# Kernel tuning notes

Measured on AMD Instinct MI355X. Metric: run time of the kernel, lower is better.

The kernel has to match this reference:

```python
import jax, jax.numpy as jnp
import numpy as np

B, N, C_IN, G = 8, 65536, 16, 64
CH = [16, 16]
EPS = 1e-3  # keras BatchNormalization default epsilon
OFFSETS = [(dx, dy, dz) for dx in (-1, 0, 1) for dy in (-1, 0, 1) for dz in (-1, 0, 1)]
G3 = G * G * G


def setup_inputs() -> dict:
    key = jax.random.key(0)
    k = jax.random.split(key, 8)
    voxel_features = jax.random.normal(k[0], (B, N, C_IN), dtype=jnp.float32)
    # unique active voxel coordinates per example (submanifold sites)
    lin = jax.vmap(lambda kk: jax.random.permutation(kk, G3)[:N])(jax.random.split(k[1], B))
    xyz = jnp.stack([lin // (G * G), (lin // G) % G, lin % G], axis=-1).astype(jnp.int32)
    num_valid_voxels = jax.random.randint(k[2], (B,), N // 2, N + 1).astype(jnp.int32)
    w0 = jax.random.uniform(k[3], (3, 3, 3, C_IN, CH[0]), minval=-0.05, maxval=0.05, dtype=jnp.float32)
    w1 = jax.random.uniform(k[4], (3, 3, 3, CH[0], CH[1]), minval=-0.05, maxval=0.05, dtype=jnp.float32)
    nw0 = jax.random.uniform(k[5], (3, 3, 3, 1, 1), minval=-0.05, maxval=0.05, dtype=jnp.float32)
    nw1 = jax.random.uniform(k[6], (3, 3, 3, 1, 1), minval=-0.05, maxval=0.05, dtype=jnp.float32)
    gamma0 = jnp.ones((CH[0],), jnp.float32); beta0 = jnp.zeros((CH[0],), jnp.float32)
    gamma1 = jnp.ones((CH[1],), jnp.float32); beta1 = jnp.zeros((CH[1],), jnp.float32)
    return dict(voxel_features=voxel_features, voxel_xyz_indices=xyz,
                num_valid_voxels=num_valid_voxels, w0=w0, w1=w1, nw0=nw0, nw1=nw1,
                gamma0=gamma0, beta0=beta0, gamma1=gamma1, beta1=beta1)


def build_neighbor_idx(coords, valid_mask):
    """For each voxel and each 3x3x3 offset, the row index of the active neighbor, or -1."""
    lin = coords[..., 0] * (G * G) + coords[..., 1] * G + coords[..., 2]  # [B,N]
    # invalid (padded) voxels write to a spare slot so they never match as neighbors
    write_lin = jnp.where(valid_mask, lin, G3 + 1)
    idx_map = jnp.full((B, G3 + 2), -1, jnp.int32)
    idx_map = idx_map.at[jnp.arange(B)[:, None], write_lin].set(
        jnp.broadcast_to(jnp.arange(N, dtype=jnp.int32)[None, :], (B, N)))
    brow = jnp.arange(B)[:, None]
    nb = []
    for dx, dy, dz in OFFSETS:
        nx = coords[..., 0] + dx; ny = coords[..., 1] + dy; nz = coords[..., 2] + dz
        inb = (nx >= 0) & (nx < G) & (ny >= 0) & (ny < G) & (nz >= 0) & (nz < G)
        nlin = jnp.where(inb, nx * (G * G) + ny * G + nz, G3)  # slot G3 always -1
        nb.append(idx_map[brow, nlin])
    return jnp.stack(nb, axis=1)  # [B,27,N]


def sparse_conv(feats, nb_idx, valid_mask, w):
    """Submanifold sparse 3D conv: output only at active sites, gathering active neighbors."""
    wf = w.reshape(27, w.shape[3], w.shape[4])  # offsets enumerate kernel taps in order
    out = jnp.zeros((feats.shape[0], feats.shape[1], w.shape[4]), feats.dtype)
    for o in range(27):
        idx = nb_idx[:, o]  # [B,N]
        g = jnp.take_along_axis(feats, jnp.maximum(idx, 0)[..., None], axis=1)
        g = jnp.where((idx >= 0)[..., None], g, 0.0)
        out = out + jnp.einsum('bnc,co->bno', g, wf[o])
    return out * valid_mask[..., None]


def masked_bn(x, valid_mask, num_valid, gamma, beta):
    m = valid_mask[..., None].astype(x.dtype)
    cnt = jnp.sum(num_valid).astype(x.dtype)
    mean = jnp.sum(x * m, axis=(0, 1)) / cnt
    var = jnp.sum(m * jnp.square(x - mean), axis=(0, 1)) / cnt
    xn = (x - mean) * jax.lax.rsqrt(var + EPS) * gamma + beta
    return xn * m  # padded rows are zero-padded, as in the TF layer


def reference(voxel_features, voxel_xyz_indices, num_valid_voxels,
              w0, w1, nw0, nw1, gamma0, beta0, gamma1, beta1):
    valid_mask = jnp.arange(N)[None, :] < num_valid_voxels[:, None]  # [B,N]
    nb_idx = build_neighbor_idx(voxel_xyz_indices, valid_mask)
    ones = jnp.ones((B, N, 1), jnp.float32)
    net = voxel_features
    for w, nw, g, b in ((w0, nw0, gamma0, beta0), (w1, nw1, gamma1, beta1)):
        net = sparse_conv(net, nb_idx, valid_mask, w)
        net_norm = sparse_conv(ones, nb_idx, valid_mask, nw)
        net = net / (1.0 + jnp.abs(net_norm))
        net = masked_bn(net, valid_mask, num_valid_voxels, g, b)
        net = jax.nn.relu(net)
    return net
```

## Files before the change

### kernel.cpp

```cpp
#include <hip/hip_runtime.h>
#include <cstdint>
#include <cstddef>

#define NB 8
#define NN 65536
#define NS (NN + 16)
#define GG 64
#define GG3 (GG*GG*GG)
#define NW (GG3/32)
#define NBLKC 2048
#define EPSC 1e-3f

typedef __bf16 bf16x8 __attribute__((ext_vector_type(8)));
typedef float  f32x4  __attribute__((ext_vector_type(4)));

__device__ __forceinline__ unsigned short f2bf(float f) {
    unsigned u = __builtin_bit_cast(unsigned, f);
    unsigned r = (u + 0x7fffu + ((u >> 16) & 1u)) >> 16;
    return (unsigned short)r;
}
__device__ __forceinline__ unsigned pk2(float a, float b) {
    return (unsigned)f2bf(a) | ((unsigned)f2bf(b) << 16);
}
__device__ __forceinline__ float bf2f(unsigned short s) {
    return __builtin_bit_cast(float, (unsigned)s << 16);
}

__device__ __forceinline__ int site_rank2(const int2* __restrict__ mwb, int lin) {
    int2 mw = mwb[lin >> 5];
    uint32_t w = (uint32_t)mw.x;
    uint32_t bit = 1u << (lin & 31);
    if (!(w & bit)) return -1;
    return mw.y + __popc(w & (bit - 1u));
}

__global__ __launch_bounds__(1024) void mask_scan_kernel(
    const int* __restrict__ xyz, const int* __restrict__ nvv,
    int2* __restrict__ mwb,
    const float* __restrict__ w0, const float* __restrict__ w1,
    unsigned short* __restrict__ wf,
    float* __restrict__ stats1, float* __restrict__ stats2)
{
    __shared__ uint32_t lmask[NW];
    __shared__ int wsum[16];
    __shared__ int woff[16];
    int b = blockIdx.x;
    int t = threadIdx.x;
    int lane = t & 63, wv = t >> 6;

    #pragma unroll
    for (int i = 0; i < NW / 1024; i++) lmask[t + i * 1024] = 0u;
    if (b == 0 && t < 512) { stats1[t] = 0.f; stats2[t] = 0.f; }
    __syncthreads();

    int cnt = nvv[b];
    const int* xb = xyz + (size_t)b * NN * 3;
    #pragma unroll 8
    for (int n = t; n < cnt; n += 1024) {
        const int* cp = xb + n * 3;
        int lin = cp[0] * (GG * GG) + cp[1] * GG + cp[2];
        atomicOr(&lmask[lin >> 5], 1u << (lin & 31));
    }
    __syncthreads();

    uint32_t wvv[8];
    int cnts[8];
    int local = 0;
    #pragma unroll
    for (int i = 0; i < 8; i++) {
        wvv[i] = lmask[i * 1024 + t];
        cnts[i] = __popc(wvv[i]);
        local += cnts[i];
    }

    int inc = local;
    #pragma unroll
    for (int d = 1; d < 64; d <<= 1) {
        int vtmp = __shfl_up(inc, d, 64);
        if (lane >= d) inc += vtmp;
    }
    if (lane == 63) wsum[wv] = inc;
    __syncthreads();
    if (t < 16) {
        int s = wsum[t];
        int e = s;
        #pragma unroll
        for (int d = 1; d < 16; d <<= 1) {
            int vtmp = __shfl_up(e, d, 16);
            if ((t & 15) >= d) e += vtmp;
        }
        woff[t] = e - s;
    }
    __syncthreads();

    int base = woff[wv] + (inc - local);
    int2* wb = mwb + (size_t)b * NW;
    #pragma unroll
    for (int i = 0; i < 8; i++) {
        wb[i * 1024 + t] = make_int2((int)wvv[i], base);
        base += cnts[i];
    }

    if (b < 2) {
        const float* w = b ? w1 : w0;
        unsigned short* o = wf + b * 14 * 512;
        for (int idx = t; idx < 14 * 512; idx += 1024) {
            int i = idx >> 9;
            int rem = idx & 511;
            int L = rem >> 3, j = rem & 7;
            int quad = L >> 4, nn = L & 15;
            int off = 2 * i + (quad >> 1);
            int c = ((quad & 1) << 3) + j;
            float v = (off < 27) ? w[(off * 16 + c) * 16 + nn] : 0.f;
            o[idx] = f2bf(v);
        }
    }
}

__global__ __launch_bounds__(256) void perm_gather_kernel(
    const int* __restrict__ xyz, const int* __restrict__ nvv,
    const int2* __restrict__ mwb,
    const float* __restrict__ feats,
    int2* __restrict__ srow,
    unsigned short* __restrict__ sfeats,
    int* __restrict__ rinv)
{
    int b = blockIdx.y;
    int n = blockIdx.x * 256 + threadIdx.x;
    int cnt = nvv[b];
    unsigned short* sfb = sfeats + (size_t)b * NS * 16;
    if (blockIdx.x == 0 && threadIdx.x < 16)
        sfb[(size_t)NN * 16 + threadIdx.x] = 0;
    if (n < cnt) {
        const int* cp = xyz + ((size_t)b * NN + n) * 3;
        int lin = cp[0] * (GG * GG) + cp[1] * GG + cp[2];
        int r = site_rank2(mwb + (size_t)b * NW, lin);
        srow[(size_t)b * NN + r] = make_int2(lin, n);
        rinv[(size_t)b * NN + n] = r;
        const float4* fp = (const float4*)(feats + ((size_t)b * NN + n) * 16);
        float4 f0 = fp[0], f1 = fp[1], f2 = fp[2], f3 = fp[3];
        uint4 lo = make_uint4(pk2(f0.x, f0.y), pk2(f0.z, f0.w),
                              pk2(f1.x, f1.y), pk2(f1.z, f1.w));
        uint4 hi = make_uint4(pk2(f2.x, f2.y), pk2(f2.z, f2.w),
                              pk2(f3.x, f3.y), pk2(f3.z, f3.w));
        *(uint4*)(sfb + (size_t)r * 16)     = lo;
        *(uint4*)(sfb + (size_t)r * 16 + 8) = hi;
    }
}

__global__ __launch_bounds__(256, 4) void conv_mfma_kernel(
    const unsigned short* __restrict__ sfeats,
    const int2*     __restrict__ srow,
    const int*      __restrict__ nvv,
    const int2*     __restrict__ mwb,
    const unsigned short* __restrict__ wfrag,
    const float*    __restrict__ nw,
    unsigned short* __restrict__ outbuf,
    float*          __restrict__ stats)
{
    int lane = threadIdx.x & 63;
    int wv = threadIdx.x >> 6;
    int m = lane & 15, quad = lane >> 4;
    int v = lane & 31, h = lane >> 5;

    int b    = blockIdx.x & 7;
    int widb = (blockIdx.x >> 3) * 4 + wv;

    __shared__ int   jj[4][32][29];
    __shared__ float rrl[4][32];
    __shared__ float red[4][32];
    __shared__ float lnw[27];

    if (threadIdx.x < 27) lnw[threadIdx.x] = nw[threadIdx.x];

    bf16x8 bfr[14];
    #pragma unroll
    for (int i = 0; i < 14; i++)
        bfr[i] = *(const bf16x8*)(wfrag + i * 512 + lane * 8);
    __syncthreads();

    float psum = 0.f, psq = 0.f;
    int coff = (quad & 1) << 3;

    int cnt = nvv[b];
    const int2* mb = mwb + (size_t)b * NW;
    const unsigned short* fb = sfeats + (size_t)b * NS * 16;
    const int2* sr = srow + (size_t)b * NN;

    int lin_nxt = sr[(widb << 5) + v].x;

    #pragma unroll 1
    for (int k = 0; k < 2; k++) {
        int r0 = (widb + k * 1024) << 5;
        int lin = lin_nxt;

        if (k == 0) {
            int Rv1 = r0 + (1024 << 5) + v;
            lin_nxt = (Rv1 < cnt) ? sr[Rv1].x : 0;
        }

        if (r0 >= cnt) continue;

        bool vld = (r0 + v) < cnt;
        if (!vld) lin = 0;
        int x = lin >> 12, y = (lin >> 6) & 63, z = lin & 63;
        int zb = z & 31;
        float nc = 0.f;
        #pragma unroll
        for (int t = 0; t < 5; t++) {
            int c = 2 * t + h;
            bool cok = c < 9;
            int cc = cok ? c : 0;
            int dx = cc / 3 - 1, dy = cc % 3 - 1;
            int nx = x + dx, ny = y + dy;
            bool colok = cok & ((unsigned)nx < 64u) & ((unsigned)ny < 64u);
            int wdi = colok ? (((nx << 12) + (ny << 6) + z) >> 5) : 0;

            int2 mw = make_int2(0, 0);
            if (vld & colok) mw = mb[wdi];
            bool need2 = vld & colok & (((zb == 0) & (z > 0)) | ((zb == 31) & (z < 63)));
            int w2 = wdi + ((zb == 0) ? -1 : 1);
            int2 mw2 = make_int2(0, 0);
            if (need2) mw2 = mb[w2];

            #pragma unroll
            for (int dz = -1; dz <= 1; dz++) {
                int zz = z + dz;
                bool zok = (unsigned)zz < 64u;
                bool same = (dz == 0) | ((dz < 0) ? (zb != 0) : (zb != 31));
                int2 word = same ? mw : mw2;
                int bb = zz & 31;
                uint32_t wm = (uint32_t)word.x;
                bool hit = vld & colok & zok & ((wm >> bb) & 1u);
                int rnk = word.y + __popc(wm & ((1u << bb) - 1u));
                int off = cc * 3 + dz + 1;
                int jv = hit ? rnk : NN;
                if (cok) {
                    jj[wv][v][off] = jv;
                    nc += hit ? lnw[off] : 0.f;
                }
            }
        }
        nc += __shfl_xor(nc, 32, 64);
        if (lane < 32) rrl[wv][v] = 1.f / (1.f + fabsf(nc));

        f32x4 acc0 = {0.f, 0.f, 0.f, 0.f};
        f32x4 acc1 = {0.f, 0.f, 0.f, 0.f};
        #pragma unroll
        for (int i = 0; i < 14; i++) {
            int off = 2 * i + (quad >> 1);
            int idx = off < 27 ? off : 28;
            int j0 = jj[wv][m][idx];      j0 = (off < 27) ? j0 : NN;
            int j1 = jj[wv][m + 16][idx]; j1 = (off < 27) ? j1 : NN;
            bf16x8 a0 = *(const bf16x8*)(fb + (size_t)j0 * 16 + coff);
            bf16x8 a1 = *(const bf16x8*)(fb + (size_t)j1 * 16 + coff);
            acc0 = __builtin_amdgcn_mfma_f32_16x16x32_bf16(a0, bfr[i], acc0, 0, 0, 0);
            acc1 = __builtin_amdgcn_mfma_f32_16x16x32_bf16(a1, bfr[i], acc1, 0, 0, 0);
        }

        #pragma unroll
        for (int hh = 0; hh < 2; hh++) {
            int rbase = r0 + (hh << 4);
            #pragma unroll
            for (int r4 = 0; r4 < 4; r4++) {
                int row = (quad << 2) + r4;
                float tval = (hh ? acc1[r4] : acc0[r4]) * rrl[wv][(hh << 4) + row];
                psum += tval; psq += tval * tval;
                int Rr = rbase + row;
                if (Rr < cnt)
                    outbuf[((size_t)b * NN + Rr) * 16 + m] = f2bf(tval);
            }
        }
    }

    psum += __shfl_xor(psum, 16, 64); psum += __shfl_xor(psum, 32, 64);
    psq  += __shfl_xor(psq, 16, 64);  psq  += __shfl_xor(psq, 32, 64);
    if (lane < 16) { red[wv][lane] = psum; red[wv][16 + lane] = psq; }
    __syncthreads();
    if (threadIdx.x < 32) {
        float vv = red[0][threadIdx.x] + red[1][threadIdx.x] +
                   red[2][threadIdx.x] + red[3][threadIdx.x];
        atomicAdd(&stats[(blockIdx.x & 15) * 32 + threadIdx.x], vv);
    }
}

__device__ __forceinline__ void compute_sb(
    const float* __restrict__ stats, const int* __restrict__ nvv,
    const float* __restrict__ gamma, const float* __restrict__ beta,
    float* sbs , float* sums )
{
    int tid = threadIdx.x;
    if (tid < 32) {
        float v = 0.f;
        #pragma unroll
        for (int s = 0; s < 16; s++) v += stats[s * 32 + tid];
        sums[tid] = v;
    }
    __syncthreads();
    if (tid < 16) {
        float cnt = 0.f;
        #pragma unroll
        for (int b = 0; b < NB; b++) cnt += (float)nvv[b];
        float mean = sums[tid] / cnt;
        float var  = fmaxf(sums[16 + tid] / cnt - mean * mean, 0.f);
        float scv = gamma[tid] * rsqrtf(var + EPSC);
        sbs[tid]      = scv;
        sbs[16 + tid] = beta[tid] - mean * scv;
    }
    __syncthreads();
}

__global__ __launch_bounds__(256) void bnrelu_sorted_kernel(
    const unsigned short* __restrict__ in, const float* __restrict__ stats,
    const int* __restrict__ nvv,
    const float* __restrict__ gamma, const float* __restrict__ beta,
    unsigned short* __restrict__ outb)
{
    __shared__ float sbs[32];
    __shared__ float sums[32];
    compute_sb(stats, nvv, gamma, beta, sbs, sums);

    int b = blockIdx.y;
    int r = blockIdx.x * 256 + threadIdx.x;
    if (r > NN) return;
    int cnt = nvv[b];
    if (r >= cnt && r != NN) return;
    uint4 lo = make_uint4(0, 0, 0, 0), hi = lo;
    if (r < cnt) {
        const uint4* ip = (const uint4*)(in + ((size_t)b * NN + r) * 16);
        uint4 xl = ip[0], xh = ip[1];
        float y[16];
        #pragma unroll
        for (int c = 0; c < 16; c++) {
            unsigned u = (c < 8) ? ((const unsigned*)&xl)[c >> 1]
                                 : ((const unsigned*)&xh)[(c - 8) >> 1];
            unsigned short sv = (c & 1) ? (unsigned short)(u >> 16)
                                        : (unsigned short)(u & 0xffff);
            y[c] = fmaxf(fmaf(bf2f(sv), sbs[c], sbs[16 + c]), 0.f);
        }
        lo = make_uint4(pk2(y[0], y[1]), pk2(y[2], y[3]), pk2(y[4], y[5]), pk2(y[6], y[7]));
        hi = make_uint4(pk2(y[8], y[9]), pk2(y[10], y[11]), pk2(y[12], y[13]), pk2(y[14], y[15]));
    }
    unsigned short* op = outb + ((size_t)b * NS + r) * 16;
    *(uint4*)op       = lo;
    *(uint4*)(op + 8) = hi;
}

__global__ __launch_bounds__(256) void final_out_kernel(
    const unsigned short* __restrict__ in,
    const int* __restrict__ rinv,
    const float* __restrict__ stats, const int* __restrict__ nvv,
    const float* __restrict__ gamma, const float* __restrict__ beta,
    float* __restrict__ out)
{
    __shared__ float sbs[32];
    __shared__ float sums[32];
    compute_sb(stats, nvv, gamma, beta, sbs, sums);

    int b = blockIdx.y;
    int n = blockIdx.x * 256 + threadIdx.x;
    int cnt = nvv[b];
    float4* op = (float4*)(out + ((size_t)b * NN + n) * 16);
    if (n < cnt) {
        int r = rinv[(size_t)b * NN + n];
        const uint4* ip = (const uint4*)(in + ((size_t)b * NN + r) * 16);
        uint4 xl = ip[0], xh = ip[1];
        float y[16];
        #pragma unroll
        for (int c = 0; c < 16; c++) {
            unsigned u = (c < 8) ? ((const unsigned*)&xl)[c >> 1]
                                 : ((const unsigned*)&xh)[(c - 8) >> 1];
            unsigned short sv = (c & 1) ? (unsigned short)(u >> 16)
                                        : (unsigned short)(u & 0xffff);
            y[c] = fmaxf(fmaf(bf2f(sv), sbs[c], sbs[16 + c]), 0.f);
        }
        op[0] = make_float4(y[0],  y[1],  y[2],  y[3]);
        op[1] = make_float4(y[4],  y[5],  y[6],  y[7]);
        op[2] = make_float4(y[8],  y[9],  y[10], y[11]);
        op[3] = make_float4(y[12], y[13], y[14], y[15]);
    } else {
        float4 z = make_float4(0.f, 0.f, 0.f, 0.f);
        op[0] = z; op[1] = z; op[2] = z; op[3] = z;
    }
}

extern "C" void kernel_launch(void* const* d_in, const int* in_sizes, int n_in,
                              void* d_out, int out_size, void* d_ws, size_t ws_size,
                              hipStream_t stream)
{
    const float* feats  = (const float*)d_in[0];
    const int*   xyz    = (const int*)d_in[1];
    const int*   nvv    = (const int*)d_in[2];
    const float* w0     = (const float*)d_in[3];
    const float* w1     = (const float*)d_in[4];
    const float* nw0    = (const float*)d_in[5];
    const float* nw1    = (const float*)d_in[6];
    const float* gamma0 = (const float*)d_in[7];
    const float* beta0  = (const float*)d_in[8];
    const float* gamma1 = (const float*)d_in[9];
    const float* beta1  = (const float*)d_in[10];
    float* out = (float*)d_out;

    char* ws = (char*)d_ws;
    float*    stats1  = (float*)ws;          ws += 16 * 32 * 4;
    float*    stats2  = (float*)ws;          ws += 16 * 32 * 4;
    int2*     mwb     = (int2*)ws;           ws += (size_t)NB * NW * 8;
    int2*     srow    = (int2*)ws;           ws += (size_t)NB * NN * 8;
    unsigned short* sfA = (unsigned short*)ws; ws += (size_t)NB * NS * 16 * 2;
    unsigned short* sfB = (unsigned short*)ws; ws += (size_t)NB * NS * 16 * 2;
    unsigned short* bufPre = (unsigned short*)ws; ws += (size_t)NB * NN * 16 * 2;
    unsigned short* wfr = (unsigned short*)ws; ws += (size_t)2 * 14 * 512 * 2;
    int*      rinv    = (int*)ws;            ws += (size_t)NB * NN * 4;

    mask_scan_kernel<<<NB, 1024, 0, stream>>>(
        xyz, nvv, mwb, w0, w1, wfr, stats1, stats2);

    dim3 gridBN(NN / 256, NB);
    perm_gather_kernel<<<gridBN, 256, 0, stream>>>(xyz, nvv, mwb, feats, srow, sfA, rinv);

    conv_mfma_kernel<<<NBLKC, 256, 0, stream>>>(
        sfA, srow, nvv, mwb, wfr, nw0, bufPre, stats1);
    bnrelu_sorted_kernel<<<dim3(NN / 256 + 1, NB), 256, 0, stream>>>(
        bufPre, stats1, nvv, gamma0, beta0, sfB);

    conv_mfma_kernel<<<NBLKC, 256, 0, stream>>>(
        sfB, srow, nvv, mwb, wfr + 14 * 512, nw1, bufPre, stats2);

    final_out_kernel<<<dim3(NN / 256, NB), 256, 0, stream>>>(
        bufPre, rinv, stats2, nvv, gamma1, beta1, out);
}
```

Before: 229.4 us.

## Fuse layer-1 BatchNorm+ReLU into the layer-2 sparse conv gather

```diff
diff --git a/kernel.cpp b/kernel.cpp
--- a/kernel.cpp
+++ b/kernel.cpp
@@ -193,12 +193,10 @@
     for (int k = 0; k < 2; k++) {
         int r0 = (widb + k * 1024) << 5;
         int lin = lin_nxt;
-
         if (k == 0) {
             int Rv1 = r0 + (1024 << 5) + v;
             lin_nxt = (Rv1 < cnt) ? sr[Rv1].x : 0;
         }
-
         if (r0 >= cnt) continue;
 
         bool vld = (r0 + v) < cnt;
@@ -310,40 +308,173 @@
     __syncthreads();
 }
 
-__global__ __launch_bounds__(256) void bnrelu_sorted_kernel(
-    const unsigned short* __restrict__ in, const float* __restrict__ stats,
-    const int* __restrict__ nvv,
-    const float* __restrict__ gamma, const float* __restrict__ beta,
-    unsigned short* __restrict__ outb)
-{
+__global__ __launch_bounds__(256, 4) void conv_mfma_bn_kernel(
+    const unsigned short* __restrict__ prebuf,
+    const int2*     __restrict__ srow,
+    const int*      __restrict__ nvv,
+    const int2*     __restrict__ mwb,
+    const unsigned short* __restrict__ wfrag,
+    const float*    __restrict__ nw,
+    const float*    __restrict__ stats1,
+    const float*    __restrict__ gamma0, const float* __restrict__ beta0,
+    unsigned short* __restrict__ outbuf,
+    float*          __restrict__ stats)
+{
+    int lane = threadIdx.x & 63;
+    int wv = threadIdx.x >> 6;
+    int m = lane & 15, quad = lane >> 4;
+    int v = lane & 31, h = lane >> 5;
+
+    int b    = blockIdx.x & 7;
+    int widb = (blockIdx.x >> 3) * 4 + wv;
+
+    __shared__ int   jj[4][32][29];
+    __shared__ float rrl[4][32];
+    __shared__ float red[4][32];
+    __shared__ float lnw[27];
     __shared__ float sbs[32];
     __shared__ float sums[32];
-    compute_sb(stats, nvv, gamma, beta, sbs, sums);
-
-    int b = blockIdx.y;
-    int r = blockIdx.x * 256 + threadIdx.x;
-    if (r > NN) return;
+
+    compute_sb(stats1, nvv, gamma0, beta0, sbs, sums);
+    if (threadIdx.x < 27) lnw[threadIdx.x] = nw[threadIdx.x];
+
+    bf16x8 bfr[14];
+    #pragma unroll
+    for (int i = 0; i < 14; i++)
+        bfr[i] = *(const bf16x8*)(wfrag + i * 512 + lane * 8);
+    __syncthreads();
+
+    int coff = (quad & 1) << 3;
+    float sreg[8], treg[8];
+    #pragma unroll
+    for (int i = 0; i < 8; i++) {
+        sreg[i] = sbs[coff + i];
+        treg[i] = sbs[16 + coff + i];
+    }
+
+    float psum = 0.f, psq = 0.f;
+
     int cnt = nvv[b];
-    if (r >= cnt && r != NN) return;
-    uint4 lo = make_uint4(0, 0, 0, 0), hi = lo;
-    if (r < cnt) {
-        const uint4* ip = (const uint4*)(in + ((size_t)b * NN + r) * 16);
-        uint4 xl = ip[0], xh = ip[1];
-        float y[16];
-        #pragma unroll
-        for (int c = 0; c < 16; c++) {
-            unsigned u = (c < 8) ? ((const unsigned*)&xl)[c >> 1]
-                                 : ((const unsigned*)&xh)[(c - 8) >> 1];
-            unsigned short sv = (c & 1) ? (unsigned short)(u >> 16)
-                                        : (unsigned short)(u & 0xffff);
-            y[c] = fmaxf(fmaf(bf2f(sv), sbs[c], sbs[16 + c]), 0.f);
-        }
-        lo = make_uint4(pk2(y[0], y[1]), pk2(y[2], y[3]), pk2(y[4], y[5]), pk2(y[6], y[7]));
-        hi = make_uint4(pk2(y[8], y[9]), pk2(y[10], y[11]), pk2(y[12], y[13]), pk2(y[14], y[15]));
-    }
-    unsigned short* op = outb + ((size_t)b * NS + r) * 16;
-    *(uint4*)op       = lo;
-    *(uint4*)(op + 8) = hi;
+    const int2* mb = mwb + (size_t)b * NW;
+    const unsigned short* pb = prebuf + (size_t)b * NN * 16;
+    const int2* sr = srow + (size_t)b * NN;
+
+    int lin_nxt = sr[(widb << 5) + v].x;
+
+    #pragma unroll 1
+    for (int k = 0; k < 2; k++) {
+        int r0 = (widb + k * 1024) << 5;
+        int lin = lin_nxt;
+        if (k == 0) {
+            int Rv1 = r0 + (1024 << 5) + v;
+            lin_nxt = (Rv1 < cnt) ? sr[Rv1].x : 0;
+        }
+        if (r0 >= cnt) continue;
+
+        bool vld = (r0 + v) < cnt;
+        if (!vld) lin = 0;
+        int x = lin >> 12, y = (lin >> 6) & 63, z = lin & 63;
+        int zb = z & 31;
+        float nc = 0.f;
+        #pragma unroll
+        for (int t = 0; t < 5; t++) {
+            int c = 2 * t + h;
+            bool cok = c < 9;
+            int cc = cok ? c : 0;
+            int dx = cc / 3 - 1, dy = cc % 3 - 1;
+            int nx = x + dx, ny = y + dy;
+            bool colok = cok & ((unsigned)nx < 64u) & ((unsigned)ny < 64u);
+            int wdi = colok ? (((nx << 12) + (ny << 6) + z) >> 5) : 0;
+
+            int2 mw = make_int2(0, 0);
+            if (vld & colok) mw = mb[wdi];
+            bool need2 = vld & colok & (((zb == 0) & (z > 0)) | ((zb == 31) & (z < 63)));
+            int w2 = wdi + ((zb == 0) ? -1 : 1);
+            int2 mw2 = make_int2(0, 0);
+            if (need2) mw2 = mb[w2];
+
+            #pragma unroll
+            for (int dz = -1; dz <= 1; dz++) {
+                int zz = z + dz;
+                bool zok = (unsigned)zz < 64u;
+                bool same = (dz == 0) | ((dz < 0) ? (zb != 0) : (zb != 31));
+                int2 word = same ? mw : mw2;
+                int bb = zz & 31;
+                uint32_t wm = (uint32_t)word.x;
+                bool hit = vld & colok & zok & ((wm >> bb) & 1u);
+                int rnk = word.y + __popc(wm & ((1u << bb) - 1u));
+                int off = cc * 3 + dz + 1;
+                int jv = hit ? rnk : NN;
+                if (cok) {
+                    jj[wv][v][off] = jv;
+                    nc += hit ? lnw[off] : 0.f;
+                }
+            }
+        }
+        nc += __shfl_xor(nc, 32, 64);
+        if (lane < 32) rrl[wv][v] = 1.f / (1.f + fabsf(nc));
+
+        f32x4 acc0 = {0.f, 0.f, 0.f, 0.f};
+        f32x4 acc1 = {0.f, 0.f, 0.f, 0.f};
+        #pragma unroll
+        for (int i = 0; i < 14; i++) {
+            int off = 2 * i + (quad >> 1);
+            int idx = off < 27 ? off : 28;
+            int j0 = jj[wv][m][idx];      j0 = (off < 27) ? j0 : NN;
+            int j1 = jj[wv][m + 16][idx]; j1 = (off < 27) ? j1 : NN;
+            uint4 u0 = *(const uint4*)(pb + (size_t)j0 * 16 + coff);
+            uint4 u1 = *(const uint4*)(pb + (size_t)j1 * 16 + coff);
+            uint4 r0v, r1v;
+            #pragma unroll
+            for (int d = 0; d < 4; d++) {
+                unsigned ua = (&u0.x)[d];
+                unsigned ub = (&u1.x)[d];
+                float a_lo = __builtin_bit_cast(float, ua << 16);
+                float a_hi = __builtin_bit_cast(float, ua & 0xffff0000u);
+                float b_lo = __builtin_bit_cast(float, ub << 16);
+                float b_hi = __builtin_bit_cast(float, ub & 0xffff0000u);
+                float ya0 = fmaxf(fmaf(a_lo, sreg[2*d],   treg[2*d]),   0.f);
+                float ya1 = fmaxf(fmaf(a_hi, sreg[2*d+1], treg[2*d+1]), 0.f);
+                float yb0 = fmaxf(fmaf(b_lo, sreg[2*d],   treg[2*d]),   0.f);
+                float yb1 = fmaxf(fmaf(b_hi, sreg[2*d+1], treg[2*d+1]), 0.f);
+                unsigned ra, rb;
+                asm("v_cvt_pk_bf16_f32 %0, %1, %2" : "=v"(ra) : "v"(ya0), "v"(ya1));
+                asm("v_cvt_pk_bf16_f32 %0, %1, %2" : "=v"(rb) : "v"(yb0), "v"(yb1));
+                (&r0v.x)[d] = ra;
+                (&r1v.x)[d] = rb;
+            }
+            if (j0 == NN) r0v = make_uint4(0, 0, 0, 0);
+            if (j1 == NN) r1v = make_uint4(0, 0, 0, 0);
+            bf16x8 a0 = __builtin_bit_cast(bf16x8, r0v);
+            bf16x8 a1 = __builtin_bit_cast(bf16x8, r1v);
+            acc0 = __builtin_amdgcn_mfma_f32_16x16x32_bf16(a0, bfr[i], acc0, 0, 0, 0);
+            acc1 = __builtin_amdgcn_mfma_f32_16x16x32_bf16(a1, bfr[i], acc1, 0, 0, 0);
+        }
+
+        #pragma unroll
+        for (int hh = 0; hh < 2; hh++) {
+            int rbase = r0 + (hh << 4);
+            #pragma unroll
+            for (int r4 = 0; r4 < 4; r4++) {
+                int row = (quad << 2) + r4;
+                float tval = (hh ? acc1[r4] : acc0[r4]) * rrl[wv][(hh << 4) + row];
+                psum += tval; psq += tval * tval;
+                int Rr = rbase + row;
+                if (Rr < cnt)
+                    outbuf[((size_t)b * NN + Rr) * 16 + m] = f2bf(tval);
+            }
+        }
+    }
+
+    psum += __shfl_xor(psum, 16, 64); psum += __shfl_xor(psum, 32, 64);
+    psq  += __shfl_xor(psq, 16, 64);  psq  += __shfl_xor(psq, 32, 64);
+    if (lane < 16) { red[wv][lane] = psum; red[wv][16 + lane] = psq; }
+    __syncthreads();
+    if (threadIdx.x < 32) {
+        float vv = red[0][threadIdx.x] + red[1][threadIdx.x] +
+                   red[2][threadIdx.x] + red[3][threadIdx.x];
+        atomicAdd(&stats[(blockIdx.x & 15) * 32 + threadIdx.x], vv);
+    }
 }
 
 __global__ __launch_bounds__(256) void final_out_kernel(
@@ -407,7 +538,7 @@
     int2*     mwb     = (int2*)ws;           ws += (size_t)NB * NW * 8;
     int2*     srow    = (int2*)ws;           ws += (size_t)NB * NN * 8;
     unsigned short* sfA = (unsigned short*)ws; ws += (size_t)NB * NS * 16 * 2;
-    unsigned short* sfB = (unsigned short*)ws; ws += (size_t)NB * NS * 16 * 2;
+    unsigned short* buf2 = (unsigned short*)ws; ws += (size_t)NB * NN * 16 * 2;
     unsigned short* bufPre = (unsigned short*)ws; ws += (size_t)NB * NN * 16 * 2;
     unsigned short* wfr = (unsigned short*)ws; ws += (size_t)2 * 14 * 512 * 2;
     int*      rinv    = (int*)ws;            ws += (size_t)NB * NN * 4;
@@ -420,12 +551,11 @@
 
     conv_mfma_kernel<<<NBLKC, 256, 0, stream>>>(
         sfA, srow, nvv, mwb, wfr, nw0, bufPre, stats1);
-    bnrelu_sorted_kernel<<<dim3(NN / 256 + 1, NB), 256, 0, stream>>>(
-        bufPre, stats1, nvv, gamma0, beta0, sfB);
-
-    conv_mfma_kernel<<<NBLKC, 256, 0, stream>>>(
-        sfB, srow, nvv, mwb, wfr + 14 * 512, nw1, bufPre, stats2);
+
+    conv_mfma_bn_kernel<<<NBLKC, 256, 0, stream>>>(
+        bufPre, srow, nvv, mwb, wfr + 14 * 512, nw1,
+        stats1, gamma0, beta0, buf2, stats2);
 
     final_out_kernel<<<dim3(NN / 256, NB), 256, 0, stream>>>(
-        bufPre, rinv, stats2, nvv, gamma1, beta1, out);
-}
+        buf2, rinv, stats2, nvv, gamma1, beta1, out);
+}
```

New measurement: 245.4 us. +7.0%, slower.
